# Performance work log

Hardware: AMD Instinct MI355X
Metric: run time of the kernel (lower is better)

Reference implementation:

```python
import jax, jax.numpy as jnp
import numpy as np

N, M, E, F = 50000, 5000, 200000, 256  # nodes, hyperedges, incidences, channels


def setup_inputs() -> dict:
    key = jax.random.key(0)
    ks = jax.random.split(key, 7)
    x = jax.random.normal(ks[0], (N, F), dtype=jnp.float32)
    hyperedge_attr = jax.random.normal(ks[1], (M, F), dtype=jnp.float32)
    # glorot-ish scale for learned params
    weight = jax.random.normal(ks[2], (F, F), dtype=jnp.float32) * (1.0 / np.sqrt(F))
    att = jax.random.normal(ks[3], (2 * F,), dtype=jnp.float32) * 0.05
    bias = jnp.zeros((F,), dtype=jnp.float32)
    node_idx = jax.random.randint(ks[4], (E,), 0, N)  # hyperedge_index[0]
    edge_idx = jax.random.randint(ks[5], (E,), 0, M)  # hyperedge_index[1]
    return {"x": x, "hyperedge_attr": hyperedge_attr, "weight": weight,
            "att": att, "bias": bias, "node_idx": node_idx, "edge_idx": edge_idx}


def reference(x, hyperedge_attr, weight, att, bias, node_idx, edge_idx):
    # HypergraphConv.forward with use_attention=True, heads=1, concat=True,
    # hyperedge_weight=None (ones), EW_weight=None, dropout=0 (eval).
    n_nodes, feat = x.shape
    n_edges = hyperedge_attr.shape[0]

    he = hyperedge_attr @ weight                       # (M, F)

    # per-incidence attention score: (cat[x_i, he_j] * att).sum(-1)
    alpha = x[node_idx] @ att[:feat] + he[edge_idx] @ att[feat:]   # (E,)
    alpha = jax.nn.leaky_relu(alpha, 0.2)
    # segment softmax over source nodes (hyperedge_index[0])
    amax = jax.lax.stop_gradient(
        jax.ops.segment_max(alpha, node_idx, num_segments=n_nodes))
    ex = jnp.exp(alpha - amax[node_idx])
    denom = jax.ops.segment_sum(ex, node_idx, num_segments=n_nodes)
    alpha = ex / denom[node_idx]                       # (E,)

    ones_e = jnp.ones((node_idx.shape[0],), dtype=x.dtype)
    # D: node degree (hyperedge_weight==1); B: hyperedge cardinality
    D = jax.ops.segment_sum(ones_e, node_idx, num_segments=n_nodes)
    Dinv = jnp.where(D > 0, 1.0 / D, 0.0)
    B = jax.ops.segment_sum(ones_e, edge_idx, num_segments=n_edges)
    Binv = jnp.where(B > 0, 1.0 / B, 0.0)

    # propagate node -> hyperedge: msg = B_i * alpha * x_j, scatter_add at edge
    msg1 = (Binv[edge_idx] * alpha)[:, None] * x[node_idx]          # (E, F)
    edge_out = jax.ops.segment_sum(msg1, edge_idx, num_segments=n_edges)  # (M, F)

    # propagate hyperedge -> node: msg = D_i * alpha * e_j, scatter_add at node
    msg2 = (Dinv[node_idx] * alpha)[:, None] * edge_out[edge_idx]   # (E, F)
    node_out = jax.ops.segment_sum(msg2, node_idx, num_segments=n_nodes)  # (N, F)

    return jax.nn.leaky_relu(node_out + bias, 0.01)
```

## Files before the change

kernel.cpp:

```cpp
#include <hip/hip_runtime.h>
#include <math.h>

#define F 256
#define NODE_STRIDE 32
#define EDGE_STRIDE 128

typedef float f32x4 __attribute__((ext_vector_type(4)));

__device__ __forceinline__ unsigned short f2bf(float f) {
    unsigned u = __float_as_uint(f);
    u = (u + 0x7FFFu + ((u >> 16) & 1u)) >> 16;
    return (unsigned short)u;
}
__device__ __forceinline__ float bf2f(unsigned short b) {
    return __uint_as_float((unsigned)b << 16);
}

__global__ void k_init_w2(const float* __restrict__ weight, const float* __restrict__ att,
                          float* __restrict__ w2,
                          float* denom, int* npos, int* epos, int N, int M) {
    int b = blockIdx.x, t = threadIdx.x;
    if (b < 64) {
        int wid = t >> 6, lane = t & 63;
        int row = b * 4 + wid;
        float4 wr = ((const float4*)(weight + (size_t)row * F))[lane];
        float4 av = ((const float4*)(att + F))[lane];
        float s = wr.x * av.x + wr.y * av.y + wr.z * av.z + wr.w * av.w;
        #pragma unroll
        for (int o = 32; o >= 1; o >>= 1) s += __shfl_down(s, o, 64);
        if (lane == 0) w2[row] = s;
    } else {
        int total = N > M ? N : M;
        int nth = (gridDim.x - 64) * blockDim.x;
        for (int i = (b - 64) * blockDim.x + t; i < total; i += nth) {
            if (i < N) { denom[i] = 0.0f; npos[i] = 0; }
            if (i < M) { epos[i] = 0; }
        }
    }
}

__global__ void k_rowdot(const float* __restrict__ x, const float* __restrict__ attr,
                         const float* __restrict__ att, const float* __restrict__ w2,
                         float* __restrict__ xa, float* __restrict__ hea,
                         unsigned short* __restrict__ xb,
                         int N, int M) {
    int wid  = (blockIdx.x * blockDim.x + threadIdx.x) >> 6;
    int lane = threadIdx.x & 63;
    if (wid >= N + M) return;
    const float* row;
    const float* vec;
    if (wid < N) { row = x    + (size_t)wid * F;       vec = att; }
    else         { row = attr + (size_t)(wid - N) * F; vec = w2;  }
    float4 rv = ((const float4*)row)[lane];
    float4 vv = ((const float4*)vec)[lane];
    if (wid < N) {
        ushort4 b4;
        b4.x = f2bf(rv.x); b4.y = f2bf(rv.y); b4.z = f2bf(rv.z); b4.w = f2bf(rv.w);
        ((ushort4*)(xb + (size_t)wid * F))[lane] = b4;
    }
    float s = rv.x * vv.x + rv.y * vv.y + rv.z * vv.z + rv.w * vv.w;
    #pragma unroll
    for (int o = 32; o >= 1; o >>= 1) s += __shfl_down(s, o, 64);
    if (lane == 0) {
        if (wid < N) xa[wid] = s;
        else         hea[wid - N] = s;
    }
}

__global__ void k_alpha_scatter(const float* __restrict__ xa, const float* __restrict__ hea,
                                const int* __restrict__ node_idx, const int* __restrict__ edge_idx,
                                float* denom, int* npos, int* epos,
                                int2* __restrict__ node_pairs, int2* __restrict__ edge_pairs,
                                int E) {
    int i = blockIdx.x * blockDim.x + threadIdx.x;
    int E4 = E >> 2;
    if (i < E4) {
        int4 nn = ((const int4*)node_idx)[i];
        int4 mm = ((const int4*)edge_idx)[i];
        float a0 = xa[nn.x] + hea[mm.x];
        float a1 = xa[nn.y] + hea[mm.y];
        float a2 = xa[nn.z] + hea[mm.z];
        float a3 = xa[nn.w] + hea[mm.w];
        a0 = a0 > 0.f ? a0 : 0.2f * a0;
        a1 = a1 > 0.f ? a1 : 0.2f * a1;
        a2 = a2 > 0.f ? a2 : 0.2f * a2;
        a3 = a3 > 0.f ? a3 : 0.2f * a3;
        float e0 = expf(a0), e1 = expf(a1), e2 = expf(a2), e3 = expf(a3);
        atomicAdd(&denom[nn.x], e0); atomicAdd(&denom[nn.y], e1);
        atomicAdd(&denom[nn.z], e2); atomicAdd(&denom[nn.w], e3);
        int p;
        p = atomicAdd(&npos[nn.x], 1); if (p < NODE_STRIDE) node_pairs[(size_t)nn.x * NODE_STRIDE + p] = make_int2(mm.x, __float_as_int(e0));
        p = atomicAdd(&npos[nn.y], 1); if (p < NODE_STRIDE) node_pairs[(size_t)nn.y * NODE_STRIDE + p] = make_int2(mm.y, __float_as_int(e1));
        p = atomicAdd(&npos[nn.z], 1); if (p < NODE_STRIDE) node_pairs[(size_t)nn.z * NODE_STRIDE + p] = make_int2(mm.z, __float_as_int(e2));
        p = atomicAdd(&npos[nn.w], 1); if (p < NODE_STRIDE) node_pairs[(size_t)nn.w * NODE_STRIDE + p] = make_int2(mm.w, __float_as_int(e3));
        p = atomicAdd(&epos[mm.x], 1); if (p < EDGE_STRIDE) edge_pairs[(size_t)mm.x * EDGE_STRIDE + p] = make_int2(nn.x, __float_as_int(e0));
        p = atomicAdd(&epos[mm.y], 1); if (p < EDGE_STRIDE) edge_pairs[(size_t)mm.y * EDGE_STRIDE + p] = make_int2(nn.y, __float_as_int(e1));
        p = atomicAdd(&epos[mm.z], 1); if (p < EDGE_STRIDE) edge_pairs[(size_t)mm.z * EDGE_STRIDE + p] = make_int2(nn.z, __float_as_int(e2));
        p = atomicAdd(&epos[mm.w], 1); if (p < EDGE_STRIDE) edge_pairs[(size_t)mm.w * EDGE_STRIDE + p] = make_int2(nn.w, __float_as_int(e3));
    } else if (i == E4) {
        for (int e = E4 * 4; e < E; ++e) {
            int n = node_idx[e], m = edge_idx[e];
            float a = xa[n] + hea[m];
            a = a > 0.f ? a : 0.2f * a;
            float ex = expf(a);
            atomicAdd(&denom[n], ex);
            int p = atomicAdd(&npos[n], 1);
            if (p < NODE_STRIDE) node_pairs[(size_t)n * NODE_STRIDE + p] = make_int2(m, __float_as_int(ex));
            int q = atomicAdd(&epos[m], 1);
            if (q < EDGE_STRIDE) edge_pairs[(size_t)m * EDGE_STRIDE + q] = make_int2(n, __float_as_int(ex));
        }
    }
}

__global__ void k_edge_gather(const unsigned short* __restrict__ xb,
                              const float* __restrict__ denom,
                              const int2* __restrict__ edge_pairs,
                              const int* __restrict__ epos,
                              unsigned short* __restrict__ edge_out, int M) {
    int m = blockIdx.x;
    if (m >= M) return;
    int wid = threadIdx.x >> 6, lane = threadIdx.x & 63;
    int B = epos[m];
    int cnt = B < EDGE_STRIDE ? B : EDGE_STRIDE;
    const int2* pairs = edge_pairs + (size_t)m * EDGE_STRIDE;
    float ax = 0.f, ay = 0.f, az = 0.f, aw = 0.f;
    for (int base = wid * 8; base < cnt; base += 32) {
        int li = base + (lane & 7);
        int2 pl = pairs[li < cnt ? li : cnt - 1];
        float wl = __int_as_float(pl.y) / denom[pl.x];
        int rem = cnt - base; if (rem > 8) rem = 8;
        #pragma unroll
        for (int j = 0; j < 8; ++j) {
            if (j < rem) {
                int   nj = __shfl(pl.x, j, 8);
                float wj = __shfl(wl,   j, 8);
                ushort4 v = ((const ushort4*)(xb + (size_t)nj * F))[lane];
                ax += wj * bf2f(v.x);
                ay += wj * bf2f(v.y);
                az += wj * bf2f(v.z);
                aw += wj * bf2f(v.w);
            }
        }
    }
    __shared__ float4 part[3][64];
    if (wid > 0) part[wid - 1][lane] = make_float4(ax, ay, az, aw);
    __syncthreads();
    if (wid == 0) {
        #pragma unroll
        for (int w = 0; w < 3; ++w) {
            float4 p = part[w][lane];
            ax += p.x; ay += p.y; az += p.z; aw += p.w;
        }
        float Binv = (B > 0) ? 1.0f / (float)B : 0.0f;
        ushort4 r;
        r.x = f2bf(ax * Binv); r.y = f2bf(ay * Binv);
        r.z = f2bf(az * Binv); r.w = f2bf(aw * Binv);
        ((ushort4*)(edge_out + (size_t)m * F))[lane] = r;
    }
}

__global__ void k_node_gather(const unsigned short* __restrict__ edge_out,
                              const int2* __restrict__ node_pairs,
                              const float* __restrict__ bias,
                              const int* __restrict__ npos,
                              const float* __restrict__ denom,
                              float* __restrict__ out, int N) {
    int n = blockIdx.x * 4 + (threadIdx.x >> 6);
    int lane = threadIdx.x & 63;
    if (n >= N) return;
    int D = npos[n];
    int cnt = D < NODE_STRIDE ? D : NODE_STRIDE;
    const int2* pairs = node_pairs + (size_t)n * NODE_STRIDE;
    float ax = 0.f, ay = 0.f, az = 0.f, aw = 0.f;
    for (int base = 0; base < cnt; base += 8) {
        int li = base + (lane & 7);
        int2 pl = pairs[li < cnt ? li : cnt - 1];
        int rem = cnt - base; if (rem > 8) rem = 8;
        #pragma unroll
        for (int j = 0; j < 8; ++j) {
            if (j < rem) {
                int   mj = __shfl(pl.x, j, 8);
                float wj = __shfl(__int_as_float(pl.y), j, 8);
                ushort4 v = ((const ushort4*)(edge_out + (size_t)mj * F))[lane];
                ax += wj * bf2f(v.x); ay += wj * bf2f(v.y);
                az += wj * bf2f(v.z); aw += wj * bf2f(v.w);
            }
        }
    }
    float scale = (D > 0) ? 1.0f / ((float)D * denom[n]) : 0.0f;
    float4 bv = ((const float4*)bias)[lane];
    f32x4 r;
    r.x = ax * scale + bv.x; r.y = ay * scale + bv.y;
    r.z = az * scale + bv.z; r.w = aw * scale + bv.w;
    r.x = r.x > 0.f ? r.x : 0.01f * r.x;
    r.y = r.y > 0.f ? r.y : 0.01f * r.y;
    r.z = r.z > 0.f ? r.z : 0.01f * r.z;
    r.w = r.w > 0.f ? r.w : 0.01f * r.w;
    __builtin_nontemporal_store(r, (f32x4*)(out + (size_t)n * F) + lane);
}

extern "C" void kernel_launch(void* const* d_in, const int* in_sizes, int n_in,
                              void* d_out, int out_size, void* d_ws, size_t ws_size,
                              hipStream_t stream) {
    const float* x        = (const float*)d_in[0];
    const float* attr     = (const float*)d_in[1];
    const float* weight   = (const float*)d_in[2];
    const float* att      = (const float*)d_in[3];
    const float* bias     = (const float*)d_in[4];
    const int*   node_idx = (const int*)d_in[5];
    const int*   edge_idx = (const int*)d_in[6];

    const int Fdim = in_sizes[4];
    const int N = in_sizes[0] / Fdim;
    const int M = in_sizes[1] / Fdim;
    const int E = in_sizes[5];
    float* out = (float*)d_out;

    char* ws = (char*)d_ws;
    auto alloc = [&](size_t bytes) -> void* {
        void* p = (void*)ws;
        ws += ((bytes + 255) / 256) * 256;
        return p;
    };
    float*          w2         = (float*)alloc((size_t)Fdim * 4);
    float*          xa         = (float*)alloc((size_t)N * 4);
    float*          hea        = (float*)alloc((size_t)M * 4);
    float*          denom      = (float*)alloc((size_t)N * 4);
    int*            npos       = (int*)alloc((size_t)N * 4);
    int*            epos       = (int*)alloc((size_t)M * 4);
    unsigned short* xb         = (unsigned short*)alloc((size_t)N * Fdim * 2);
    int2*           node_pairs = (int2*)alloc((size_t)N * NODE_STRIDE * 8);
    int2*           edge_pairs = (int2*)alloc((size_t)M * EDGE_STRIDE * 8);
    unsigned short* edge_out   = (unsigned short*)alloc((size_t)M * Fdim * 2);

    hipLaunchKernelGGL(k_init_w2, dim3(256), dim3(256), 0, stream,
                       weight, att, w2, denom, npos, epos, N, M);
    int rows = N + M;
    hipLaunchKernelGGL(k_rowdot, dim3((rows + 3) / 4), dim3(256), 0, stream,
                       x, attr, att, w2, xa, hea, xb, N, M);
    int E4 = E / 4;
    hipLaunchKernelGGL(k_alpha_scatter, dim3((E4 + 1 + 255) / 256), dim3(256), 0, stream,
                       xa, hea, node_idx, edge_idx, denom, npos, epos,
                       node_pairs, edge_pairs, E);
    hipLaunchKernelGGL(k_edge_gather, dim3(M), dim3(256), 0, stream,
                       xb, denom, edge_pairs, epos, edge_out, M);
    hipLaunchKernelGGL(k_node_gather, dim3((N + 3) / 4), dim3(256), 0, stream,
                       edge_out, node_pairs, bias, npos, denom, out, N);
}
```

Measured before the change: 108.7 us.

## Use 16-byte bf16 row loads with half-wave split and persistent grids in gathers

Both gather kernels now split each wave into two 32-lane halves. Each lane loads 8 bf16 values (16 bytes) instead of 4, and each half processes a different incidence, so two rows are in flight per instruction. The halves are combined with a cross-half shuffle. The launches switch to grid-stride loops with capped grid sizes (2048 blocks), which amortises block setup but adds per-iteration __syncthreads in the edge kernel and can reduce latency hiding.

```diff
diff --git a/kernel.cpp b/kernel.cpp
--- a/kernel.cpp
+++ b/kernel.cpp
@@ -6,6 +6,7 @@
 #define EDGE_STRIDE 128
 
 typedef float f32x4 __attribute__((ext_vector_type(4)));
+typedef unsigned short u16x8 __attribute__((ext_vector_type(8)));
 
 __device__ __forceinline__ unsigned short f2bf(float f) {
     unsigned u = __float_as_uint(f);
@@ -117,45 +118,50 @@
                               const int2* __restrict__ edge_pairs,
                               const int* __restrict__ epos,
                               unsigned short* __restrict__ edge_out, int M) {
-    int m = blockIdx.x;
-    if (m >= M) return;
     int wid = threadIdx.x >> 6, lane = threadIdx.x & 63;
-    int B = epos[m];
-    int cnt = B < EDGE_STRIDE ? B : EDGE_STRIDE;
-    const int2* pairs = edge_pairs + (size_t)m * EDGE_STRIDE;
-    float ax = 0.f, ay = 0.f, az = 0.f, aw = 0.f;
-    for (int base = wid * 8; base < cnt; base += 32) {
-        int li = base + (lane & 7);
-        int2 pl = pairs[li < cnt ? li : cnt - 1];
-        float wl = __int_as_float(pl.y) / denom[pl.x];
-        int rem = cnt - base; if (rem > 8) rem = 8;
+    int half = lane >> 5, fl = lane & 31;
+    __shared__ float part[3][32][8];
+    for (int m = blockIdx.x; m < M; m += gridDim.x) {
+        int B = epos[m];
+        int cnt = B < EDGE_STRIDE ? B : EDGE_STRIDE;
+        const int2* pairs = edge_pairs + (size_t)m * EDGE_STRIDE;
+        float acc[8] = {0.f, 0.f, 0.f, 0.f, 0.f, 0.f, 0.f, 0.f};
+        for (int base = wid * 16; base < cnt; base += 64) {
+            int li = base + (lane & 15);
+            int2 pl = pairs[li < cnt ? li : cnt - 1];
+            float wl = __int_as_float(pl.y) / denom[pl.x];
+            int rem = cnt - base; if (rem > 16) rem = 16;
+            #pragma unroll
+            for (int k = 0; k < 8; ++k) {
+                int pi = 2 * k + half;
+                if (pi < rem) {
+                    int   nj = __shfl(pl.x, pi, 16);
+                    float wj = __shfl(wl,   pi, 16);
+                    u16x8 v = ((const u16x8*)(xb + (size_t)nj * F))[fl];
+                    #pragma unroll
+                    for (int q = 0; q < 8; ++q) acc[q] += wj * bf2f(v[q]);
+                }
+            }
+        }
         #pragma unroll
-        for (int j = 0; j < 8; ++j) {
-            if (j < rem) {
-                int   nj = __shfl(pl.x, j, 8);
-                float wj = __shfl(wl,   j, 8);
-                ushort4 v = ((const ushort4*)(xb + (size_t)nj * F))[lane];
-                ax += wj * bf2f(v.x);
-                ay += wj * bf2f(v.y);
-                az += wj * bf2f(v.z);
-                aw += wj * bf2f(v.w);
-            }
-        }
-    }
-    __shared__ float4 part[3][64];
-    if (wid > 0) part[wid - 1][lane] = make_float4(ax, ay, az, aw);
-    __syncthreads();
-    if (wid == 0) {
-        #pragma unroll
-        for (int w = 0; w < 3; ++w) {
-            float4 p = part[w][lane];
-            ax += p.x; ay += p.y; az += p.z; aw += p.w;
-        }
-        float Binv = (B > 0) ? 1.0f / (float)B : 0.0f;
-        ushort4 r;
-        r.x = f2bf(ax * Binv); r.y = f2bf(ay * Binv);
-        r.z = f2bf(az * Binv); r.w = f2bf(aw * Binv);
-        ((ushort4*)(edge_out + (size_t)m * F))[lane] = r;
+        for (int q = 0; q < 8; ++q) acc[q] += __shfl_xor(acc[q], 32, 64);
+        if (wid > 0 && half == 0) {
+            #pragma unroll
+            for (int q = 0; q < 8; ++q) part[wid - 1][fl][q] = acc[q];
+        }
+        __syncthreads();
+        if (wid == 0 && half == 0) {
+            #pragma unroll
+            for (int w = 0; w < 3; ++w)
+                #pragma unroll
+                for (int q = 0; q < 8; ++q) acc[q] += part[w][fl][q];
+            float Binv = (B > 0) ? 1.0f / (float)B : 0.0f;
+            u16x8 r;
+            #pragma unroll
+            for (int q = 0; q < 8; ++q) r[q] = f2bf(acc[q] * Binv);
+            ((u16x8*)(edge_out + (size_t)m * F))[fl] = r;
+        }
+        __syncthreads();
     }
 }
 
@@ -165,38 +171,53 @@
                               const int* __restrict__ npos,
                               const float* __restrict__ denom,
                               float* __restrict__ out, int N) {
-    int n = blockIdx.x * 4 + (threadIdx.x >> 6);
-    int lane = threadIdx.x & 63;
-    if (n >= N) return;
-    int D = npos[n];
-    int cnt = D < NODE_STRIDE ? D : NODE_STRIDE;
-    const int2* pairs = node_pairs + (size_t)n * NODE_STRIDE;
-    float ax = 0.f, ay = 0.f, az = 0.f, aw = 0.f;
-    for (int base = 0; base < cnt; base += 8) {
-        int li = base + (lane & 7);
-        int2 pl = pairs[li < cnt ? li : cnt - 1];
-        int rem = cnt - base; if (rem > 8) rem = 8;
+    int wid = threadIdx.x >> 6, lane = threadIdx.x & 63;
+    int half = lane >> 5, fl = lane & 31;
+    f32x4 b0 = ((const f32x4*)bias)[fl * 2];
+    f32x4 b1 = ((const f32x4*)bias)[fl * 2 + 1];
+    for (int n = blockIdx.x * 4 + wid; n < N; n += gridDim.x * 4) {
+        int D = npos[n];
+        int cnt = D < NODE_STRIDE ? D : NODE_STRIDE;
+        const int2* pairs = node_pairs + (size_t)n * NODE_STRIDE;
+        float acc[8] = {0.f, 0.f, 0.f, 0.f, 0.f, 0.f, 0.f, 0.f};
+        for (int base = 0; base < cnt; base += 16) {
+            int li = base + (lane & 15);
+            int2 pl = pairs[li < cnt ? li : cnt - 1];
+            float wl = __int_as_float(pl.y);
+            int rem = cnt - base; if (rem > 16) rem = 16;
+            #pragma unroll
+            for (int k = 0; k < 8; ++k) {
+                int pi = 2 * k + half;
+                if (pi < rem) {
+                    int   mj = __shfl(pl.x, pi, 16);
+                    float wj = __shfl(wl,   pi, 16);
+                    u16x8 v = ((const u16x8*)(edge_out + (size_t)mj * F))[fl];
+                    #pragma unroll
+                    for (int q = 0; q < 8; ++q) acc[q] += wj * bf2f(v[q]);
+                }
+            }
+        }
         #pragma unroll
-        for (int j = 0; j < 8; ++j) {
-            if (j < rem) {
-                int   mj = __shfl(pl.x, j, 8);
-                float wj = __shfl(__int_as_float(pl.y), j, 8);
-                ushort4 v = ((const ushort4*)(edge_out + (size_t)mj * F))[lane];
-                ax += wj * bf2f(v.x); ay += wj * bf2f(v.y);
-                az += wj * bf2f(v.z); aw += wj * bf2f(v.w);
-            }
-        }
-    }
-    float scale = (D > 0) ? 1.0f / ((float)D * denom[n]) : 0.0f;
-    float4 bv = ((const float4*)bias)[lane];
-    f32x4 r;
-    r.x = ax * scale + bv.x; r.y = ay * scale + bv.y;
-    r.z = az * scale + bv.z; r.w = aw * scale + bv.w;
-    r.x = r.x > 0.f ? r.x : 0.01f * r.x;
-    r.y = r.y > 0.f ? r.y : 0.01f * r.y;
-    r.z = r.z > 0.f ? r.z : 0.01f * r.z;
-    r.w = r.w > 0.f ? r.w : 0.01f * r.w;
-    __builtin_nontemporal_store(r, (f32x4*)(out + (size_t)n * F) + lane);
+        for (int q = 0; q < 8; ++q) acc[q] += __shfl_xor(acc[q], 32, 64);
+        if (half == 0) {
+            float scale = (D > 0) ? 1.0f / ((float)D * denom[n]) : 0.0f;
+            f32x4 r0, r1;
+            r0.x = acc[0] * scale + b0.x; r0.y = acc[1] * scale + b0.y;
+            r0.z = acc[2] * scale + b0.z; r0.w = acc[3] * scale + b0.w;
+            r1.x = acc[4] * scale + b1.x; r1.y = acc[5] * scale + b1.y;
+            r1.z = acc[6] * scale + b1.z; r1.w = acc[7] * scale + b1.w;
+            r0.x = r0.x > 0.f ? r0.x : 0.01f * r0.x;
+            r0.y = r0.y > 0.f ? r0.y : 0.01f * r0.y;
+            r0.z = r0.z > 0.f ? r0.z : 0.01f * r0.z;
+            r0.w = r0.w > 0.f ? r0.w : 0.01f * r0.w;
+            r1.x = r1.x > 0.f ? r1.x : 0.01f * r1.x;
+            r1.y = r1.y > 0.f ? r1.y : 0.01f * r1.y;
+            r1.z = r1.z > 0.f ? r1.z : 0.01f * r1.z;
+            r1.w = r1.w > 0.f ? r1.w : 0.01f * r1.w;
+            __builtin_nontemporal_store(r0, (f32x4*)(out + (size_t)n * F) + fl * 2);
+            __builtin_nontemporal_store(r1, (f32x4*)(out + (size_t)n * F) + fl * 2 + 1);
+        }
+    }
 }
 
 extern "C" void kernel_launch(void* const* d_in, const int* in_sizes, int n_in,
@@ -242,8 +263,10 @@
     hipLaunchKernelGGL(k_alpha_scatter, dim3((E4 + 1 + 255) / 256), dim3(256), 0, stream,
                        xa, hea, node_idx, edge_idx, denom, npos, epos,
                        node_pairs, edge_pairs, E);
-    hipLaunchKernelGGL(k_edge_gather, dim3(M), dim3(256), 0, stream,
+    int egrid = M < 2048 ? M : 2048;
+    hipLaunchKernelGGL(k_edge_gather, dim3(egrid), dim3(256), 0, stream,
                        xb, denom, edge_pairs, epos, edge_out, M);
-    hipLaunchKernelGGL(k_node_gather, dim3((N + 3) / 4), dim3(256), 0, stream,
+    int ngrid = 2048;
+    hipLaunchKernelGGL(k_node_gather, dim3(ngrid), dim3(256), 0, stream,
                        edge_out, node_pairs, bias, npos, denom, out, N);
 }
```

Result: faster. 97.60 us (-10.2%).
